# Optimization experiments

Measured on AMD Instinct MI355X. Metric: run time of the kernel, lower is better.

The kernel has to match this reference:

```python
import jax, jax.numpy as jnp
import numpy as np

EPS = 1e-5      # BatchNorm2d default eps
SLOPE = 0.01    # F.leaky_relu default negative slope


def _bn(h, gamma, beta):
    # training-mode BatchNorm2d with batch=1: normalize per channel over the
    # N x N spatial extent (channels are the last axis here).
    mean = jnp.mean(h, axis=(0, 1))
    var = jnp.var(h, axis=(0, 1))  # biased variance, as torch uses for normalization
    return (h - mean) * jax.lax.rsqrt(var + EPS) * gamma + beta


def _block(h, W, b, gamma, beta):
    # 1x1 conv == per-position channel matmul; layout [N, N, C]
    h = jnp.einsum('nmc,oc->nmo', h, W) + b
    return jax.nn.leaky_relu(_bn(h, gamma, beta), SLOPE)


def setup_inputs() -> dict:
    key = jax.random.key(0)
    ks = jax.random.split(key, 12)
    N, C = 1536, 64
    H = [16, 16, 8, 8]  # nf * ratio
    x = jax.random.normal(ks[0], (N, C), dtype=jnp.float32)
    def w(k, o, i):
        return jax.random.normal(k, (o, i), dtype=jnp.float32) * (1.0 / np.sqrt(i))
    inp = {
        'x': x,
        'W1': w(ks[1], H[0], C),   'b1': jnp.zeros((H[0],), jnp.float32),
        'g1': jnp.ones((H[0],), jnp.float32), 'be1': jnp.zeros((H[0],), jnp.float32),
        'W2': w(ks[2], H[1], H[0]), 'b2': jnp.zeros((H[1],), jnp.float32),
        'g2': jnp.ones((H[1],), jnp.float32), 'be2': jnp.zeros((H[1],), jnp.float32),
        'W3': w(ks[3], H[2], H[1]), 'b3': jnp.zeros((H[2],), jnp.float32),
        'g3': jnp.ones((H[2],), jnp.float32), 'be3': jnp.zeros((H[2],), jnp.float32),
        'W4': w(ks[4], H[3], H[2]), 'b4': jnp.zeros((H[3],), jnp.float32),
        'g4': jnp.ones((H[3],), jnp.float32), 'be4': jnp.zeros((H[3],), jnp.float32),
        'W5': w(ks[5], 1, H[3]),    'b5': jnp.zeros((1,), jnp.float32),
    }
    return inp


def reference(x, W1, b1, g1, be1, W2, b2, g2, be2, W3, b3, g3, be3,
              W4, b4, g4, be4, W5, b5):
    # pairwise abs-diff adjacency features: [N, N, C]
    adj = jnp.abs(x[:, None, :] - x[None, :, :])
    h = _block(adj, W1, b1, g1, be1)
    h = _block(h, W2, b2, g2, be2)
    h = _block(h, W3, b3, g3, be3)
    h = _block(h, W4, b4, g4, be4)
    out = jnp.einsum('nmc,oc->nmo', h, W5) + b5  # [N, N, 1]
    return out[..., 0]  # [N, N]
```

## Files before the change

### kernel.cpp

```cpp
#include <hip/hip_runtime.h>
#include <stdint.h>


#define NPTS 1536
#define NTILES 4656
#define NBLK 256
#define NTMAX 19
static constexpr float FNN   = 2359296.0f;
static constexpr float EPS   = 1e-5f;
static constexpr float SLOPE = 0.01f;
static constexpr float INV_M = 1.0f / 2359296.0f;

typedef __attribute__((ext_vector_type(8)))  short bf16x8;
typedef __attribute__((ext_vector_type(4)))  float f32x4;
typedef __attribute__((ext_vector_type(16))) float f32x16;
union frag8 { int4 i; bf16x8 v; };

__device__ __forceinline__ float bflo(unsigned u) {
    return __builtin_bit_cast(float, u << 16);
}
__device__ __forceinline__ float bfhi(unsigned u) {
    return __builtin_bit_cast(float, u & 0xffff0000u);
}
__device__ __forceinline__ unsigned short f2bf(float f) {
    unsigned u = __builtin_bit_cast(unsigned, f);
    u += 0x7fffu + ((u >> 16) & 1u);
    return (unsigned short)(u >> 16);
}
__device__ __forceinline__ unsigned pack2(float lo, float hi) {
    return (unsigned)f2bf(lo) | ((unsigned)f2bf(hi) << 16);
}
__device__ __forceinline__ unsigned packtr(float lo, float hi) {
    unsigned a = __builtin_bit_cast(unsigned, lo);
    unsigned b = __builtin_bit_cast(unsigned, hi);
#if __has_builtin(__builtin_amdgcn_perm)
    return __builtin_amdgcn_perm(b, a, 0x07060302u);
#else
    return (a >> 16) | (b & 0xffff0000u);
#endif
}
__device__ __forceinline__ float lrelu(float t) {
    return fmaxf(t, t * SLOPE);
}
__device__ __forceinline__ float4 ld4(const float* p) {
    return *(const float4*)p;
}
__device__ __forceinline__ unsigned shflx32(unsigned v) {
    return (unsigned)__shfl_xor((int)v, 32);
}
__device__ __forceinline__ float aload(const float* p) {
    int vi = __hip_atomic_load((const int*)p, __ATOMIC_RELAXED,
                               __HIP_MEMORY_SCOPE_AGENT);
    return __builtin_bit_cast(float, vi);
}

__device__ __forceinline__ void gbar(int* flags, int epoch) {
    __syncthreads();
    if (threadIdx.x == 0) {
        asm volatile("s_waitcnt vmcnt(0)" ::: "memory");
        __hip_atomic_store(flags + (int)blockIdx.x * 16, epoch,
                           __ATOMIC_RELAXED, __HIP_MEMORY_SCOPE_AGENT);
    }
    if (threadIdx.x < 256) {
        const int* f = flags + (int)threadIdx.x * 16;
        while (__hip_atomic_load(f, __ATOMIC_RELAXED,
                                 __HIP_MEMORY_SCOPE_AGENT) < epoch) {
            __builtin_amdgcn_s_sleep(2);
        }
    }
    __syncthreads();
}

__device__ __forceinline__ int2 tri_decode(int t) {
    float disc = 37249.0f - 8.0f * (float)t;
    int mt = (int)((193.0f - sqrtf(disc)) * 0.5f);
    if (mt < 0) mt = 0;
    if (mt > 95) mt = 95;
    while (96 * (mt + 1) - ((mt + 1) * mt) / 2 <= t) mt++;
    while (96 * mt - (mt * (mt - 1)) / 2 > t) mt--;
    int nc = mt + (t - (96 * mt - (mt * (mt - 1)) / 2));
    return make_int2(mt, nc);
}

__device__ __forceinline__ void bn8_inline(
        const float* stats, const float* __restrict__ g,
        const float* __restrict__ be, float* sc, float* sh) {
#pragma unroll
    for (int c = 0; c < 8; c++) {
        float S = 0.f, Q = 0.f;
#pragma unroll
        for (int rp = 0; rp < 16; rp++) {
            S += stats[rp * 16 + c];
            Q += stats[rp * 16 + 8 + c];
        }
        float mu  = S * INV_M;
        float var = fmaf(-mu, mu, Q * INV_M);
        float s   = g[c] * rsqrtf(var + EPS);
        sc[c] = s;
        sh[c] = fmaf(-mu, s, be[c]);
    }
}

__global__ __launch_bounds__(256) void k_prep(float* __restrict__ ws) {
    int t = blockIdx.x * 256 + threadIdx.x;
    if (t < 5632) ws[t] = 0.0f;
}

struct TSet {
    float4 a0, a1, a2, a3;
    float4 p0, p1, p2, p3;
    float4 q0, q1, q2, q3;
};

__global__ __launch_bounds__(512, 2) void k_mega(
        const float* __restrict__ x,
        const float* __restrict__ W1, const float* __restrict__ b1,
        const float* __restrict__ g1, const float* __restrict__ be1,
        const float* __restrict__ W2, const float* __restrict__ b2,
        const float* __restrict__ g2, const float* __restrict__ be2,
        const float* __restrict__ W3, const float* __restrict__ b3,
        const float* __restrict__ g3, const float* __restrict__ be3,
        const float* __restrict__ W4, const float* __restrict__ b4,
        const float* __restrict__ g4, const float* __restrict__ be4,
        const float* __restrict__ W5, const float* __restrict__ b5,
        float* __restrict__ out, float* __restrict__ ws) {

    __shared__ unsigned short hbuf[NTMAX * 4096];
    __shared__ float red[8][32];
    __shared__ float Tm[2][2][272];
    __shared__ int tdesc[NTMAX + 1];
    __shared__ float sstat[512];

    int tid  = threadIdx.x;
    int bid  = blockIdx.x;
    int w    = tid >> 6;
    int lane = tid & 63;
    int NT   = 18 + (bid < 48 ? 1 : 0);

    float* stats1 = ws;
    float* raw2   = ws + 512;
    float* stats3 = ws + 1024;
    float* stats4 = ws + 1280;
    int* flags    = (int*)(ws + 1536);
    int rep32 = (bid & 15) * 32;
    int rep16 = (bid & 15) * 16;

    if (tid < NT) {
        int2 tc = tri_decode(bid + NBLK * tid);
        tdesc[tid] = (tc.x << 8) | tc.y;
    }
    __syncthreads();
    if (w == 0) {
        bool dg = false;
        if (lane < NT) {
            int td = tdesc[lane];
            dg = (td >> 8) == (td & 255);
        }
        unsigned long long m = __ballot(dg);
        if (lane == 0) tdesc[NTMAX] = (int)(unsigned)m;
    }
    __syncthreads();
    unsigned diagmask = (unsigned)tdesc[NTMAX];

    {
        int l15 = lane & 15, quad = lane >> 4, cb = quad * 8;
        const float* wr = W1 + l15 * 64 + cb;
        float4 w0 = ld4(wr);
        float4 w1v = ld4(wr + 4);
        float4 w2v = ld4(wr + 32);
        float4 w3v = ld4(wr + 36);
        frag8 fb1, fb2;
        fb1.i = make_int4(pack2(w0.x, w0.y), pack2(w0.z, w0.w),
                          pack2(w1v.x, w1v.y), pack2(w1v.z, w1v.w));
        fb2.i = make_int4(pack2(w2v.x, w2v.y), pack2(w2v.z, w2v.w),
                          pack2(w3v.x, w3v.y), pack2(w3v.z, w3v.w));
        float4 b1v = ld4(b1 + quad * 4);
        float lsum[4] = {0.f, 0.f, 0.f, 0.f};
        float lssq[4] = {0.f, 0.f, 0.f, 0.f};

        auto loadT = [&](int i, TSet& s) {
            int td = tdesc[i];
            int mt = td >> 8, nc = td & 255;
            const float* xr = x + (mt * 16 + l15) * 64 + cb;
            s.a0 = ld4(xr); s.a1 = ld4(xr + 4);
            s.a2 = ld4(xr + 32); s.a3 = ld4(xr + 36);
            const float* pA = x + (size_t)(nc * 16 + 2 * w) * 64 + cb;
            s.p0 = ld4(pA); s.p1 = ld4(pA + 4);
            s.p2 = ld4(pA + 32); s.p3 = ld4(pA + 36);
            const float* pB = x + (size_t)(nc * 16 + 2 * w + 1) * 64 + cb;
            s.q0 = ld4(pB); s.q1 = ld4(pB + 4);
            s.q2 = ld4(pB + 32); s.q3 = ld4(pB + 36);
        };
        auto colT = [&](int i, float wf, int j, float4 u0, float4 u1,
                        float4 u2, float4 u3, const TSet& s) {
            frag8 fa1, fa2;
            fa1.i = make_int4(
                packtr(fabsf(s.a0.x - u0.x), fabsf(s.a0.y - u0.y)),
                packtr(fabsf(s.a0.z - u0.z), fabsf(s.a0.w - u0.w)),
                packtr(fabsf(s.a1.x - u1.x), fabsf(s.a1.y - u1.y)),
                packtr(fabsf(s.a1.z - u1.z), fabsf(s.a1.w - u1.w)));
            fa2.i = make_int4(
                packtr(fabsf(s.a2.x - u2.x), fabsf(s.a2.y - u2.y)),
                packtr(fabsf(s.a2.z - u2.z), fabsf(s.a2.w - u2.w)),
                packtr(fabsf(s.a3.x - u3.x), fabsf(s.a3.y - u3.y)),
                packtr(fabsf(s.a3.z - u3.z), fabsf(s.a3.w - u3.w)));
            f32x4 acc = {b1v.x, b1v.y, b1v.z, b1v.w};
            acc = __builtin_amdgcn_mfma_f32_16x16x32_bf16(fb1.v, fa1.v,
                                                          acc, 0, 0, 0);
            acc = __builtin_amdgcn_mfma_f32_16x16x32_bf16(fb2.v, fa2.v,
                                                          acc, 0, 0, 0);
#pragma unroll
            for (int r = 0; r < 4; r++) {
                float wa = wf * acc[r];
                lsum[r] += wa;
                lssq[r] = fmaf(wa, acc[r], lssq[r]);
            }
            *(uint2*)(hbuf + i * 4096 + j * 256 + l15 * 16 + quad * 4) =
                make_uint2(pack2(acc[0], acc[1]), pack2(acc[2], acc[3]));
        };
        auto computeT = [&](int i, const TSet& s) {
            float wf = ((diagmask >> i) & 1u) ? 1.0f : 2.0f;
            colT(i, wf, 2 * w,     s.p0, s.p1, s.p2, s.p3, s);
            colT(i, wf, 2 * w + 1, s.q0, s.q1, s.q2, s.q3, s);
        };

        TSet A, B;
        loadT(0, A);
        int i = 0;
#pragma unroll 1
        for (; i + 2 <= NT; i += 2) {
            loadT(i + 1, B);
            computeT(i, A);
            if (i + 2 < NT) loadT(i + 2, A);
            computeT(i + 1, B);
        }
        if (i < NT) computeT(i, A);

#pragma unroll
        for (int off = 1; off < 16; off <<= 1) {
#pragma unroll
            for (int r = 0; r < 4; r++) {
                lsum[r] += __shfl_xor(lsum[r], off);
                lssq[r] += __shfl_xor(lssq[r], off);
            }
        }
        if (l15 == 0) {
#pragma unroll
            for (int r = 0; r < 4; r++) {
                red[w][quad * 4 + r]      = lsum[r];
                red[w][16 + quad * 4 + r] = lssq[r];
            }
        }
        __syncthreads();
        if (tid < 32) {
            float v = 0.f;
#pragma unroll
            for (int k = 0; k < 8; k++) v += red[k][tid];
            atomicAdd(stats1 + rep32 + tid, v);
        }
    }
    gbar(flags, 1);
    sstat[tid] = aload(stats1 + tid);
    __syncthreads();

    {
        int pc = lane & 31, kh = lane >> 5;
        float sc[8], sh[8];
#pragma unroll
        for (int jc = 0; jc < 8; jc++) {
            int c = kh * 8 + jc;
            float S = 0.f, Q = 0.f;
#pragma unroll
            for (int rp = 0; rp < 16; rp++) {
                S += sstat[rp * 32 + c];
                Q += sstat[rp * 32 + 16 + c];
            }
            float mu  = S * INV_M;
            float var = fmaf(-mu, mu, Q * INV_M);
            float s   = g1[c] * rsqrtf(var + EPS);
            sc[jc] = s;
            sh[jc] = fmaf(-mu, s, be1[c]);
        }
        frag8 fw2; fw2.i = make_int4(0, 0, 0, 0);
        if (pc < 16) {
            const float* wp = W2 + pc * 16 + kh * 8;
            float4 wa = ld4(wp), wb = ld4(wp + 4);
            fw2.i = make_int4(pack2(wa.x, wa.y), pack2(wa.z, wa.w),
                              pack2(wb.x, wb.y), pack2(wb.z, wb.w));
        }
        f32x16 z;
#pragma unroll
        for (int r = 0; r < 16; r++) z[r] = 0.0f;
        float sum2[8], ssq2[8];
#pragma unroll
        for (int r = 0; r < 8; r++) { sum2[r] = 0.f; ssq2[r] = 0.f; }

        int base = w * 512 + pc * 16 + kh * 8;

        auto body2 = [&](int i, uint4 v) {
            float wf = ((diagmask >> i) & 1u) ? 1.0f : 2.0f;
            float a0 = bflo(v.x), a1 = bfhi(v.x);
            float a2 = bflo(v.y), a3 = bfhi(v.y);
            float a4 = bflo(v.z), a5 = bfhi(v.z);
            float a6 = bflo(v.w), a7 = bfhi(v.w);
            a0 = lrelu(fmaf(a0, sc[0], sh[0]));
            a1 = lrelu(fmaf(a1, sc[1], sh[1]));
            a2 = lrelu(fmaf(a2, sc[2], sh[2]));
            a3 = lrelu(fmaf(a3, sc[3], sh[3]));
            a4 = lrelu(fmaf(a4, sc[4], sh[4]));
            a5 = lrelu(fmaf(a5, sc[5], sh[5]));
            a6 = lrelu(fmaf(a6, sc[6], sh[6]));
            a7 = lrelu(fmaf(a7, sc[7], sh[7]));
            frag8 fbv;
            fbv.i = make_int4(packtr(a0, a1), packtr(a2, a3),
                              packtr(a4, a5), packtr(a6, a7));
            *(uint4*)(hbuf + i * 4096 + base) =
                make_uint4(fbv.i.x, fbv.i.y, fbv.i.z, fbv.i.w);
            f32x16 d = __builtin_amdgcn_mfma_f32_32x32x16_bf16(fw2.v, fbv.v,
                                                               z, 0, 0, 0);
#pragma unroll
            for (int r = 0; r < 8; r++) {
                float dv = d[r];
                float wd = wf * dv;
                sum2[r] += wd;
                ssq2[r] = fmaf(wd, dv, ssq2[r]);
            }
        };

        uint4 v0 = *(const uint4*)(hbuf + base);
        uint4 v1 = *(const uint4*)(hbuf + 4096 + base);
        int i = 0;
#pragma unroll 1
        for (; i + 2 <= NT; i += 2) {
            uint4 n0 = v0, n1 = v1;
            if (i + 3 < NT) {
                n0 = *(const uint4*)(hbuf + (i + 2) * 4096 + base);
                n1 = *(const uint4*)(hbuf + (i + 3) * 4096 + base);
            } else if (i + 2 < NT) {
                n0 = *(const uint4*)(hbuf + (i + 2) * 4096 + base);
            }
            body2(i, v0);
            body2(i + 1, v1);
            v0 = n0; v1 = n1;
        }
        if (i < NT) body2(i, v0);

#pragma unroll
        for (int off = 1; off < 32; off <<= 1) {
#pragma unroll
            for (int r = 0; r < 8; r++) {
                sum2[r] += __shfl_xor(sum2[r], off);
                ssq2[r] += __shfl_xor(ssq2[r], off);
            }
        }
        if (pc == 0) {
#pragma unroll
            for (int r = 0; r < 8; r++) {
                int o = (r & 3) + 8 * (r >> 2) + 4 * kh;
                red[w][o]      = sum2[r];
                red[w][16 + o] = ssq2[r];
            }
        }
        __syncthreads();
        if (tid < 32) {
            float v = 0.f;
#pragma unroll
            for (int k = 0; k < 8; k++) v += red[k][tid];
            atomicAdd(raw2 + rep32 + tid, v);
        }
    }
    gbar(flags, 2);
    sstat[tid] = aload(raw2 + tid);
    __syncthreads();

    {
        int pc = lane & 31, kh = lane >> 5;
        float sc2[8], sh2[8];
#pragma unroll
        for (int r = 0; r < 8; r++) {
            int c = (r & 3) + 8 * (r >> 2) + 4 * kh;
            float S = 0.f, Q = 0.f;
#pragma unroll
            for (int rp = 0; rp < 16; rp++) {
                S += sstat[rp * 32 + c];
                Q += sstat[rp * 32 + 16 + c];
            }
            float bc = b2[c];
            float sm = S + FNN * bc;
            float sq = Q + 2.0f * bc * S + FNN * bc * bc;
            float mu  = sm * INV_M;
            float var = fmaf(-mu, mu, sq * INV_M);
            float s   = g2[c] * rsqrtf(var + EPS);
            float shv = fmaf(-mu, s, be2[c]);
            sc2[r] = s;
            sh2[r] = fmaf(s, bc, shv);
        }
        frag8 fw2; fw2.i = make_int4(0, 0, 0, 0);
        if (pc < 16) {
            const float* wp = W2 + pc * 16 + kh * 8;
            float4 wa = ld4(wp), wb = ld4(wp + 4);
            fw2.i = make_int4(pack2(wa.x, wa.y), pack2(wa.z, wa.w),
                              pack2(wb.x, wb.y), pack2(wb.z, wb.w));
        }
        frag8 fw3; fw3.i = make_int4(0, 0, 0, 0);
        if (pc < 8) {
            const float* wp = W3 + pc * 16 + kh * 8;
            float4 wa = ld4(wp), wb = ld4(wp + 4);
            fw3.i = make_int4(pack2(wa.x, wa.y), pack2(wa.z, wa.w),
                              pack2(wb.x, wb.y), pack2(wb.z, wb.w));
        }
        float b3r[4];
#pragma unroll
        for (int r = 0; r < 4; r++) b3r[r] = b3[kh * 4 + r];
        f32x16 z;
#pragma unroll
        for (int r = 0; r < 16; r++) z[r] = 0.0f;
        float sum3[4] = {0.f, 0.f, 0.f, 0.f};
        float ssq3[4] = {0.f, 0.f, 0.f, 0.f};

        int rbase = w * 512 + pc * 16 + kh * 8;
        int wbase = w * 512 + pc * 8 + kh * 4;

        uint4 v = *(const uint4*)(hbuf + rbase);
#pragma unroll 1
        for (int i = 0; i < NT; i++) {
            uint4 vn = v;
            if (i + 1 < NT)
                vn = *(const uint4*)(hbuf + (i + 1) * 4096 + rbase);
            float wf = ((diagmask >> i) & 1u) ? 1.0f : 2.0f;
            frag8 fbv;
            fbv.i = make_int4((int)v.x, (int)v.y, (int)v.z, (int)v.w);
            f32x16 d = __builtin_amdgcn_mfma_f32_32x32x16_bf16(fw2.v, fbv.v,
                                                               z, 0, 0, 0);
            float t0 = lrelu(fmaf(d[0], sc2[0], sh2[0]));
            float t1 = lrelu(fmaf(d[1], sc2[1], sh2[1]));
            float t2 = lrelu(fmaf(d[2], sc2[2], sh2[2]));
            float t3 = lrelu(fmaf(d[3], sc2[3], sh2[3]));
            float t4 = lrelu(fmaf(d[4], sc2[4], sh2[4]));
            float t5 = lrelu(fmaf(d[5], sc2[5], sh2[5]));
            float t6 = lrelu(fmaf(d[6], sc2[6], sh2[6]));
            float t7 = lrelu(fmaf(d[7], sc2[7], sh2[7]));
            unsigned e0 = packtr(t0, t1), e1 = packtr(t2, t3);
            unsigned e2 = packtr(t4, t5), e3 = packtr(t6, t7);
            unsigned p0 = kh ? e0 : e2;
            unsigned p1 = kh ? e1 : e3;
            unsigned q0 = shflx32(p0);
            unsigned q1 = shflx32(p1);
            frag8 fb2;
            fb2.i = make_int4(kh ? q0 : e0, kh ? q1 : e1,
                              kh ? e2 : q0, kh ? e3 : q1);
            f32x16 d2 = __builtin_amdgcn_mfma_f32_32x32x16_bf16(fw3.v, fb2.v,
                                                                z, 0, 0, 0);
            float h0  = d2[0] + b3r[0];
            float h1v = d2[1] + b3r[1];
            float h2v = d2[2] + b3r[2];
            float h3v = d2[3] + b3r[3];
            float wh;
            wh = wf * h0;  sum3[0] += wh; ssq3[0] = fmaf(wh, h0,  ssq3[0]);
            wh = wf * h1v; sum3[1] += wh; ssq3[1] = fmaf(wh, h1v, ssq3[1]);
            wh = wf * h2v; sum3[2] += wh; ssq3[2] = fmaf(wh, h2v, ssq3[2]);
            wh = wf * h3v; sum3[3] += wh; ssq3[3] = fmaf(wh, h3v, ssq3[3]);
            *(uint2*)(hbuf + i * 4096 + wbase) =
                make_uint2(pack2(h0, h1v), pack2(h2v, h3v));
            v = vn;
        }
#pragma unroll
        for (int off = 1; off < 32; off <<= 1) {
#pragma unroll
            for (int r = 0; r < 4; r++) {
                sum3[r] += __shfl_xor(sum3[r], off);
                ssq3[r] += __shfl_xor(ssq3[r], off);
            }
        }
        if (pc == 0) {
#pragma unroll
            for (int r = 0; r < 4; r++) {
                red[w][kh * 4 + r]     = sum3[r];
                red[w][8 + kh * 4 + r] = ssq3[r];
            }
        }
        __syncthreads();
        if (tid < 16) {
            float v2 = 0.f;
#pragma unroll
            for (int k = 0; k < 8; k++) v2 += red[k][tid];
            atomicAdd(stats3 + rep16 + tid, v2);
        }
    }
    gbar(flags, 3);
    if (tid < 256) sstat[tid] = aload(stats3 + tid);
    __syncthreads();

    {
        float sc3[8], sh3[8];
        bn8_inline(sstat, g3, be3, sc3, sh3);
        int h = tid >> 8;
        int p = tid & 255;
        int pbase = (p >> 5) * 512 + (p & 31) * 8;

        float w4r[8][8], bi[8];
#pragma unroll
        for (int o = 0; o < 8; o++) {
            const float* wr = W4 + o * 8;
            float4 v0 = ld4(wr);
            float4 v1 = ld4(wr + 4);
            w4r[o][0] = v0.x; w4r[o][1] = v0.y;
            w4r[o][2] = v0.z; w4r[o][3] = v0.w;
            w4r[o][4] = v1.x; w4r[o][5] = v1.y;
            w4r[o][6] = v1.z; w4r[o][7] = v1.w;
            bi[o] = b4[o];
        }
        float sum4[8], ssq4[8];
#pragma unroll
        for (int o = 0; o < 8; o++) { sum4[o] = 0.f; ssq4[o] = 0.f; }

        uint4 v = *(const uint4*)(hbuf + h * 4096 + pbase);
#pragma unroll 1
        for (int i = h; i < NT; i += 2) {
            uint4 vn = v;
            if (i + 2 < NT)
                vn = *(const uint4*)(hbuf + (i + 2) * 4096 + pbase);
            float wf = ((diagmask >> i) & 1u) ? 1.0f : 2.0f;
            float a0 = bflo(v.x), a1 = bfhi(v.x);
            float a2 = bflo(v.y), a3 = bfhi(v.y);
            float a4 = bflo(v.z), a5 = bfhi(v.z);
            float a6 = bflo(v.w), a7 = bfhi(v.w);
            a0 = lrelu(fmaf(a0, sc3[0], sh3[0]));
            a1 = lrelu(fmaf(a1, sc3[1], sh3[1]));
            a2 = lrelu(fmaf(a2, sc3[2], sh3[2]));
            a3 = lrelu(fmaf(a3, sc3[3], sh3[3]));
            a4 = lrelu(fmaf(a4, sc3[4], sh3[4]));
            a5 = lrelu(fmaf(a5, sc3[5], sh3[5]));
            a6 = lrelu(fmaf(a6, sc3[6], sh3[6]));
            a7 = lrelu(fmaf(a7, sc3[7], sh3[7]));
            uint4 pk = make_uint4(pack2(a0, a1), pack2(a2, a3),
                                  pack2(a4, a5), pack2(a6, a7));
            *(uint4*)(hbuf + i * 4096 + pbase) = pk;
            float r[8];
            r[0] = bflo(pk.x); r[1] = bfhi(pk.x);
            r[2] = bflo(pk.y); r[3] = bfhi(pk.y);
            r[4] = bflo(pk.z); r[5] = bfhi(pk.z);
            r[6] = bflo(pk.w); r[7] = bfhi(pk.w);
            float d[8];
#pragma unroll
            for (int o = 0; o < 8; o++) d[o] = bi[o];
#pragma unroll
            for (int c = 0; c < 8; c++) {
#pragma unroll
                for (int o = 0; o < 8; o++)
                    d[o] = fmaf(r[c], w4r[o][c], d[o]);
            }
#pragma unroll
            for (int o = 0; o < 8; o++) {
                float wd = wf * d[o];
                sum4[o] += wd;
                ssq4[o] = fmaf(wd, d[o], ssq4[o]);
            }
            v = vn;
        }
#pragma unroll
        for (int off = 1; off < 64; off <<= 1) {
#pragma unroll
            for (int o = 0; o < 8; o++) {
                sum4[o] += __shfl_xor(sum4[o], off);
                ssq4[o] += __shfl_xor(ssq4[o], off);
            }
        }
        if (lane == 0) {
#pragma unroll
            for (int o = 0; o < 8; o++) {
                red[w][o]     = sum4[o];
                red[w][8 + o] = ssq4[o];
            }
        }
        __syncthreads();
        if (tid < 16) {
            float v2 = 0.f;
#pragma unroll
            for (int k = 0; k < 8; k++) v2 += red[k][tid];
            atomicAdd(stats4 + rep16 + tid, v2);
        }
    }
    gbar(flags, 4);
    if (tid < 256) sstat[tid] = aload(stats4 + tid);
    __syncthreads();

    {
        float w4f[8][8], b4f[8], w5r[8];
#pragma unroll
        for (int o = 0; o < 8; o++) {
            float S = 0.f, Q = 0.f;
#pragma unroll
            for (int rp = 0; rp < 16; rp++) {
                S += sstat[rp * 16 + o];
                Q += sstat[rp * 16 + 8 + o];
            }
            float mu  = S * INV_M;
            float var = fmaf(-mu, mu, Q * INV_M);
            float s   = g4[o] * rsqrtf(var + EPS);
            float shv = fmaf(-mu, s, be4[o]);
            b4f[o] = fmaf(s, b4[o], shv);
            const float* wr = W4 + o * 8;
            float4 v0 = ld4(wr);
            float4 v1 = ld4(wr + 4);
            w4f[o][0] = s * v0.x; w4f[o][1] = s * v0.y;
            w4f[o][2] = s * v0.z; w4f[o][3] = s * v0.w;
            w4f[o][4] = s * v1.x; w4f[o][5] = s * v1.y;
            w4f[o][6] = s * v1.z; w4f[o][7] = s * v1.w;
            w5r[o] = W5[o];
        }
        float b5v = b5[0];
        int half = tid >> 8;
        int lt   = tid & 255;
        int nl = lt >> 4, ml = lt & 15;
        int pbase = (lt >> 5) * 512 + (lt & 31) * 8;
        int npair = (NT + 1) >> 1;
        int buf = 0;

#pragma unroll 1
        for (int jp = 0; jp < npair; jp++) {
            int i = 2 * jp + half;
            bool act = (i < NT);
            int mt = 0, nc = 0;
            if (act) {
                int td = tdesc[i];
                mt = td >> 8; nc = td & 255;
                uint4 v = *(const uint4*)(hbuf + i * 4096 + pbase);
                float a[8];
                a[0] = bflo(v.x); a[1] = bfhi(v.x);
                a[2] = bflo(v.y); a[3] = bfhi(v.y);
                a[4] = bflo(v.z); a[5] = bfhi(v.z);
                a[6] = bflo(v.w); a[7] = bfhi(v.w);
                float accv = b5v;
#pragma unroll
                for (int o = 0; o < 8; o++) {
                    float hh = b4f[o];
#pragma unroll
                    for (int c = 0; c < 8; c++)
                        hh = fmaf(a[c], w4f[o][c], hh);
                    accv = fmaf(lrelu(hh), w5r[o], accv);
                }
                out[(size_t)(nc * 16 + nl) * NPTS + mt * 16 + ml] = accv;
                Tm[buf][half][nl * 17 + ml] = accv;
            }
            __syncthreads();
            if (act) {
                float mv = Tm[buf][half][ml * 17 + nl];
                out[(size_t)(mt * 16 + nl) * NPTS + nc * 16 + ml] = mv;
            }
            buf ^= 1;
        }
    }
}

extern "C" void kernel_launch(void* const* d_in, const int* in_sizes, int n_in,
                              void* d_out, int out_size, void* d_ws,
                              size_t ws_size, hipStream_t stream) {
    const float* x   = (const float*)d_in[0];
    const float* W1  = (const float*)d_in[1];
    const float* b1  = (const float*)d_in[2];
    const float* g1  = (const float*)d_in[3];
    const float* be1 = (const float*)d_in[4];
    const float* W2  = (const float*)d_in[5];
    const float* b2  = (const float*)d_in[6];
    const float* g2  = (const float*)d_in[7];
    const float* be2 = (const float*)d_in[8];
    const float* W3  = (const float*)d_in[9];
    const float* b3  = (const float*)d_in[10];
    const float* g3  = (const float*)d_in[11];
    const float* be3 = (const float*)d_in[12];
    const float* W4  = (const float*)d_in[13];
    const float* b4  = (const float*)d_in[14];
    const float* g4  = (const float*)d_in[15];
    const float* be4 = (const float*)d_in[16];
    const float* W5  = (const float*)d_in[17];
    const float* b5  = (const float*)d_in[18];

    float* ws   = (float*)d_ws;
    float* outp = (float*)d_out;

    k_prep<<<22, 256, 0, stream>>>(ws);
    k_mega<<<NBLK, 512, 0, stream>>>(
        x, W1, b1, g1, be1, W2, b2, g2, be2, W3, b3, g3, be3,
        W4, b4, g4, be4, W5, b5, outp, ws);
}
```

Before: 174.6 us.

## Widen mega-kernel blocks to 768 threads with strided per-wave task distribution

Raises the block size from 512 to 768 threads (12 waves) and rewrites every stage's loop to spread flattened (tile, column/chunk) tasks across waves with a stride of 12 and two-deep register prefetch. The aim is more waves per CU to hide latency while the LDS-resident tile buffer stays the same. The final stage now runs three tile groups per round and needs an extra barrier per round, since its transpose buffer is no longer double-buffered. Launch bounds drop to 768x3, which tightens the per-thread register budget and may cause spills.

```diff
diff --git a/kernel.cpp b/kernel.cpp
--- a/kernel.cpp
+++ b/kernel.cpp
@@ -106,13 +106,12 @@
     if (t < 5632) ws[t] = 0.0f;
 }
 
-struct TSet {
+struct TSet1 {
     float4 a0, a1, a2, a3;
-    float4 p0, p1, p2, p3;
-    float4 q0, q1, q2, q3;
+    float4 u0, u1, u2, u3;
 };
 
-__global__ __launch_bounds__(512, 2) void k_mega(
+__global__ __launch_bounds__(768, 3) void k_mega(
         const float* __restrict__ x,
         const float* __restrict__ W1, const float* __restrict__ b1,
         const float* __restrict__ g1, const float* __restrict__ be1,
@@ -126,8 +125,8 @@
         float* __restrict__ out, float* __restrict__ ws) {
 
     __shared__ unsigned short hbuf[NTMAX * 4096];
-    __shared__ float red[8][32];
-    __shared__ float Tm[2][2][272];
+    __shared__ float red[12][32];
+    __shared__ float Tm[3][272];
     __shared__ int tdesc[NTMAX + 1];
     __shared__ float sstat[512];
 
@@ -177,33 +176,33 @@
         float4 b1v = ld4(b1 + quad * 4);
         float lsum[4] = {0.f, 0.f, 0.f, 0.f};
         float lssq[4] = {0.f, 0.f, 0.f, 0.f};
-
-        auto loadT = [&](int i, TSet& s) {
+        int NTASK = NT * 16;
+
+        auto loadT = [&](int t, TSet1& s) {
+            int i = t >> 4, j = t & 15;
             int td = tdesc[i];
             int mt = td >> 8, nc = td & 255;
             const float* xr = x + (mt * 16 + l15) * 64 + cb;
             s.a0 = ld4(xr); s.a1 = ld4(xr + 4);
             s.a2 = ld4(xr + 32); s.a3 = ld4(xr + 36);
-            const float* pA = x + (size_t)(nc * 16 + 2 * w) * 64 + cb;
-            s.p0 = ld4(pA); s.p1 = ld4(pA + 4);
-            s.p2 = ld4(pA + 32); s.p3 = ld4(pA + 36);
-            const float* pB = x + (size_t)(nc * 16 + 2 * w + 1) * 64 + cb;
-            s.q0 = ld4(pB); s.q1 = ld4(pB + 4);
-            s.q2 = ld4(pB + 32); s.q3 = ld4(pB + 36);
+            const float* xp = x + (size_t)(nc * 16 + j) * 64 + cb;
+            s.u0 = ld4(xp); s.u1 = ld4(xp + 4);
+            s.u2 = ld4(xp + 32); s.u3 = ld4(xp + 36);
         };
-        auto colT = [&](int i, float wf, int j, float4 u0, float4 u1,
-                        float4 u2, float4 u3, const TSet& s) {
+        auto computeT = [&](int t, const TSet1& s) {
+            int i = t >> 4, j = t & 15;
+            float wf = ((diagmask >> i) & 1u) ? 1.0f : 2.0f;
             frag8 fa1, fa2;
             fa1.i = make_int4(
-                packtr(fabsf(s.a0.x - u0.x), fabsf(s.a0.y - u0.y)),
-                packtr(fabsf(s.a0.z - u0.z), fabsf(s.a0.w - u0.w)),
-                packtr(fabsf(s.a1.x - u1.x), fabsf(s.a1.y - u1.y)),
-                packtr(fabsf(s.a1.z - u1.z), fabsf(s.a1.w - u1.w)));
+                packtr(fabsf(s.a0.x - s.u0.x), fabsf(s.a0.y - s.u0.y)),
+                packtr(fabsf(s.a0.z - s.u0.z), fabsf(s.a0.w - s.u0.w)),
+                packtr(fabsf(s.a1.x - s.u1.x), fabsf(s.a1.y - s.u1.y)),
+                packtr(fabsf(s.a1.z - s.u1.z), fabsf(s.a1.w - s.u1.w)));
             fa2.i = make_int4(
-                packtr(fabsf(s.a2.x - u2.x), fabsf(s.a2.y - u2.y)),
-                packtr(fabsf(s.a2.z - u2.z), fabsf(s.a2.w - u2.w)),
-                packtr(fabsf(s.a3.x - u3.x), fabsf(s.a3.y - u3.y)),
-                packtr(fabsf(s.a3.z - u3.z), fabsf(s.a3.w - u3.w)));
+                packtr(fabsf(s.a2.x - s.u2.x), fabsf(s.a2.y - s.u2.y)),
+                packtr(fabsf(s.a2.z - s.u2.z), fabsf(s.a2.w - s.u2.w)),
+                packtr(fabsf(s.a3.x - s.u3.x), fabsf(s.a3.y - s.u3.y)),
+                packtr(fabsf(s.a3.z - s.u3.z), fabsf(s.a3.w - s.u3.w)));
             f32x4 acc = {b1v.x, b1v.y, b1v.z, b1v.w};
             acc = __builtin_amdgcn_mfma_f32_16x16x32_bf16(fb1.v, fa1.v,
                                                           acc, 0, 0, 0);
@@ -218,23 +217,20 @@
             *(uint2*)(hbuf + i * 4096 + j * 256 + l15 * 16 + quad * 4) =
                 make_uint2(pack2(acc[0], acc[1]), pack2(acc[2], acc[3]));
         };
-        auto computeT = [&](int i, const TSet& s) {
-            float wf = ((diagmask >> i) & 1u) ? 1.0f : 2.0f;
-            colT(i, wf, 2 * w,     s.p0, s.p1, s.p2, s.p3, s);
-            colT(i, wf, 2 * w + 1, s.q0, s.q1, s.q2, s.q3, s);
-        };
-
-        TSet A, B;
-        loadT(0, A);
-        int i = 0;
+
+        TSet1 A, B;
+        int t = w;
+        loadT(t, A);
+        if (t + 12 < NTASK) loadT(t + 12, B);
 #pragma unroll 1
-        for (; i + 2 <= NT; i += 2) {
-            loadT(i + 1, B);
-            computeT(i, A);
-            if (i + 2 < NT) loadT(i + 2, A);
-            computeT(i + 1, B);
-        }
-        if (i < NT) computeT(i, A);
+        for (; t < NTASK; t += 24) {
+            computeT(t, A);
+            if (t + 24 < NTASK) loadT(t + 24, A);
+            if (t + 12 < NTASK) {
+                computeT(t + 12, B);
+                if (t + 36 < NTASK) loadT(t + 36, B);
+            }
+        }
 
 #pragma unroll
         for (int off = 1; off < 16; off <<= 1) {
@@ -255,12 +251,12 @@
         if (tid < 32) {
             float v = 0.f;
 #pragma unroll
-            for (int k = 0; k < 8; k++) v += red[k][tid];
+            for (int k = 0; k < 12; k++) v += red[k][tid];
             atomicAdd(stats1 + rep32 + tid, v);
         }
     }
     gbar(flags, 1);
-    sstat[tid] = aload(stats1 + tid);
+    if (tid < 512) sstat[tid] = aload(stats1 + tid);
     __syncthreads();
 
     {
@@ -295,9 +291,13 @@
 #pragma unroll
         for (int r = 0; r < 8; r++) { sum2[r] = 0.f; ssq2[r] = 0.f; }
 
-        int base = w * 512 + pc * 16 + kh * 8;
-
-        auto body2 = [&](int i, uint4 v) {
+        int NT8 = NT * 8;
+        int lanebase = pc * 16 + kh * 8;
+        auto addr2 = [&](int t) {
+            return (t >> 3) * 4096 + (t & 7) * 512 + lanebase;
+        };
+        auto body2 = [&](int t, uint4 v) {
+            int i = t >> 3;
             float wf = ((diagmask >> i) & 1u) ? 1.0f : 2.0f;
             float a0 = bflo(v.x), a1 = bfhi(v.x);
             float a2 = bflo(v.y), a3 = bfhi(v.y);
@@ -314,7 +314,7 @@
             frag8 fbv;
             fbv.i = make_int4(packtr(a0, a1), packtr(a2, a3),
                               packtr(a4, a5), packtr(a6, a7));
-            *(uint4*)(hbuf + i * 4096 + base) =
+            *(uint4*)(hbuf + addr2(t)) =
                 make_uint4(fbv.i.x, fbv.i.y, fbv.i.z, fbv.i.w);
             f32x16 d = __builtin_amdgcn_mfma_f32_32x32x16_bf16(fw2.v, fbv.v,
                                                                z, 0, 0, 0);
@@ -327,23 +327,19 @@
             }
         };
 
-        uint4 v0 = *(const uint4*)(hbuf + base);
-        uint4 v1 = *(const uint4*)(hbuf + 4096 + base);
-        int i = 0;
+        int t = w;
+        uint4 v0 = *(const uint4*)(hbuf + addr2(t));
+        uint4 v1 = make_uint4(0, 0, 0, 0);
+        if (t + 12 < NT8) v1 = *(const uint4*)(hbuf + addr2(t + 12));
 #pragma unroll 1
-        for (; i + 2 <= NT; i += 2) {
+        for (; t < NT8; t += 24) {
             uint4 n0 = v0, n1 = v1;
-            if (i + 3 < NT) {
-                n0 = *(const uint4*)(hbuf + (i + 2) * 4096 + base);
-                n1 = *(const uint4*)(hbuf + (i + 3) * 4096 + base);
-            } else if (i + 2 < NT) {
-                n0 = *(const uint4*)(hbuf + (i + 2) * 4096 + base);
-            }
-            body2(i, v0);
-            body2(i + 1, v1);
+            if (t + 24 < NT8) n0 = *(const uint4*)(hbuf + addr2(t + 24));
+            if (t + 36 < NT8) n1 = *(const uint4*)(hbuf + addr2(t + 36));
+            body2(t, v0);
+            if (t + 12 < NT8) body2(t + 12, v1);
             v0 = n0; v1 = n1;
         }
-        if (i < NT) body2(i, v0);
 
 #pragma unroll
         for (int off = 1; off < 32; off <<= 1) {
@@ -365,12 +361,12 @@
         if (tid < 32) {
             float v = 0.f;
 #pragma unroll
-            for (int k = 0; k < 8; k++) v += red[k][tid];
+            for (int k = 0; k < 12; k++) v += red[k][tid];
             atomicAdd(raw2 + rep32 + tid, v);
         }
     }
     gbar(flags, 2);
-    sstat[tid] = aload(raw2 + tid);
+    if (tid < 512) sstat[tid] = aload(raw2 + tid);
     __syncthreads();
 
     {
@@ -418,15 +414,14 @@
         float sum3[4] = {0.f, 0.f, 0.f, 0.f};
         float ssq3[4] = {0.f, 0.f, 0.f, 0.f};
 
-        int rbase = w * 512 + pc * 16 + kh * 8;
-        int wbase = w * 512 + pc * 8 + kh * 4;
-
-        uint4 v = *(const uint4*)(hbuf + rbase);
-#pragma unroll 1
-        for (int i = 0; i < NT; i++) {
-            uint4 vn = v;
-            if (i + 1 < NT)
-                vn = *(const uint4*)(hbuf + (i + 1) * 4096 + rbase);
+        int NT8 = NT * 8;
+        int rlane = pc * 16 + kh * 8;
+        int wlane = pc * 8 + kh * 4;
+        auto raddr = [&](int t) {
+            return (t >> 3) * 4096 + (t & 7) * 512 + rlane;
+        };
+        auto body3 = [&](int t, uint4 v) {
+            int i = t >> 3, ck = t & 7;
             float wf = ((diagmask >> i) & 1u) ? 1.0f : 2.0f;
             frag8 fbv;
             fbv.i = make_int4((int)v.x, (int)v.y, (int)v.z, (int)v.w);
@@ -460,10 +455,24 @@
             wh = wf * h1v; sum3[1] += wh; ssq3[1] = fmaf(wh, h1v, ssq3[1]);
             wh = wf * h2v; sum3[2] += wh; ssq3[2] = fmaf(wh, h2v, ssq3[2]);
             wh = wf * h3v; sum3[3] += wh; ssq3[3] = fmaf(wh, h3v, ssq3[3]);
-            *(uint2*)(hbuf + i * 4096 + wbase) =
+            *(uint2*)(hbuf + i * 4096 + ck * 512 + wlane) =
                 make_uint2(pack2(h0, h1v), pack2(h2v, h3v));
-            v = vn;
-        }
+        };
+
+        int t = w;
+        uint4 v0 = *(const uint4*)(hbuf + raddr(t));
+        uint4 v1 = make_uint4(0, 0, 0, 0);
+        if (t + 12 < NT8) v1 = *(const uint4*)(hbuf + raddr(t + 12));
+#pragma unroll 1
+        for (; t < NT8; t += 24) {
+            uint4 n0 = v0, n1 = v1;
+            if (t + 24 < NT8) n0 = *(const uint4*)(hbuf + raddr(t + 24));
+            if (t + 36 < NT8) n1 = *(const uint4*)(hbuf + raddr(t + 36));
+            body3(t, v0);
+            if (t + 12 < NT8) body3(t + 12, v1);
+            v0 = n0; v1 = n1;
+        }
+
 #pragma unroll
         for (int off = 1; off < 32; off <<= 1) {
 #pragma unroll
@@ -483,7 +492,7 @@
         if (tid < 16) {
             float v2 = 0.f;
 #pragma unroll
-            for (int k = 0; k < 8; k++) v2 += red[k][tid];
+            for (int k = 0; k < 12; k++) v2 += red[k][tid];
             atomicAdd(stats3 + rep16 + tid, v2);
         }
     }
@@ -494,7 +503,7 @@
     {
         float sc3[8], sh3[8];
         bn8_inline(sstat, g3, be3, sc3, sh3);
-        int h = tid >> 8;
+        int g = tid >> 8;
         int p = tid & 255;
         int pbase = (p >> 5) * 512 + (p & 31) * 8;
 
@@ -514,12 +523,7 @@
 #pragma unroll
         for (int o = 0; o < 8; o++) { sum4[o] = 0.f; ssq4[o] = 0.f; }
 
-        uint4 v = *(const uint4*)(hbuf + h * 4096 + pbase);
-#pragma unroll 1
-        for (int i = h; i < NT; i += 2) {
-            uint4 vn = v;
-            if (i + 2 < NT)
-                vn = *(const uint4*)(hbuf + (i + 2) * 4096 + pbase);
+        auto body4 = [&](int i, uint4 v) {
             float wf = ((diagmask >> i) & 1u) ? 1.0f : 2.0f;
             float a0 = bflo(v.x), a1 = bfhi(v.x);
             float a2 = bflo(v.y), a3 = bfhi(v.y);
@@ -556,7 +560,23 @@
                 sum4[o] += wd;
                 ssq4[o] = fmaf(wd, d[o], ssq4[o]);
             }
-            v = vn;
+        };
+
+        uint4 v0 = *(const uint4*)(hbuf + g * 4096 + pbase);
+        uint4 v1 = make_uint4(0, 0, 0, 0);
+        if (g + 3 < NT)
+            v1 = *(const uint4*)(hbuf + (g + 3) * 4096 + pbase);
+        int i = g;
+#pragma unroll 1
+        for (; i < NT; i += 6) {
+            uint4 n0 = v0, n1 = v1;
+            if (i + 6 < NT)
+                n0 = *(const uint4*)(hbuf + (i + 6) * 4096 + pbase);
+            if (i + 9 < NT)
+                n1 = *(const uint4*)(hbuf + (i + 9) * 4096 + pbase);
+            body4(i, v0);
+            if (i + 3 < NT) body4(i + 3, v1);
+            v0 = n0; v1 = n1;
         }
 #pragma unroll
         for (int off = 1; off < 64; off <<= 1) {
@@ -577,7 +597,7 @@
         if (tid < 16) {
             float v2 = 0.f;
 #pragma unroll
-            for (int k = 0; k < 8; k++) v2 += red[k][tid];
+            for (int k = 0; k < 12; k++) v2 += red[k][tid];
             atomicAdd(stats4 + rep16 + tid, v2);
         }
     }
@@ -610,16 +630,15 @@
             w5r[o] = W5[o];
         }
         float b5v = b5[0];
-        int half = tid >> 8;
-        int lt   = tid & 255;
+        int g  = tid >> 8;
+        int lt = tid & 255;
         int nl = lt >> 4, ml = lt & 15;
         int pbase = (lt >> 5) * 512 + (lt & 31) * 8;
-        int npair = (NT + 1) >> 1;
-        int buf = 0;
+        int nround = (NT + 2) / 3;
 
 #pragma unroll 1
-        for (int jp = 0; jp < npair; jp++) {
-            int i = 2 * jp + half;
+        for (int jp = 0; jp < nround; jp++) {
+            int i = 3 * jp + g;
             bool act = (i < NT);
             int mt = 0, nc = 0;
             if (act) {
@@ -641,14 +660,14 @@
                     accv = fmaf(lrelu(hh), w5r[o], accv);
                 }
                 out[(size_t)(nc * 16 + nl) * NPTS + mt * 16 + ml] = accv;
-                Tm[buf][half][nl * 17 + ml] = accv;
+                Tm[g][nl * 17 + ml] = accv;
             }
             __syncthreads();
             if (act) {
-                float mv = Tm[buf][half][ml * 17 + nl];
+                float mv = Tm[g][ml * 17 + nl];
                 out[(size_t)(mt * 16 + nl) * NPTS + nc * 16 + ml] = mv;
             }
-            buf ^= 1;
+            __syncthreads();
         }
     }
 }
@@ -680,7 +699,7 @@
     float* outp = (float*)d_out;
 
     k_prep<<<22, 256, 0, stream>>>(ws);
-    k_mega<<<NBLK, 512, 0, stream>>>(
+    k_mega<<<NBLK, 768, 0, stream>>>(
         x, W1, b1, g1, be1, W2, b2, g2, be2, W3, b3, g3, be3,
         W4, b4, g4, be4, W5, b5, outp, ws);
 }
```

Measured after the change: 244.6 us. +40.1%, slower.
